# Kernel tuning notes

Measured on AMD Instinct MI355X. Metric: run time of the kernel, lower is better.

## Reference

```python
import jax, jax.numpy as jnp
import numpy as np

N = 10000       # n_nodes
E = 640000      # n_edges (avg degree 64)
D_IN = 128      # in_feats
D_H = 128       # n_hidden
N_CLS = 64      # n_classes


def setup_inputs() -> dict:
    key = jax.random.key(0)
    k1, k2, k3, k4, k5, k6 = jax.random.split(key, 6)
    features = jax.random.normal(k1, (N, D_IN), dtype=jnp.float32)
    src = jax.random.randint(k2, (E,), 0, N, dtype=jnp.int32)
    dst = jax.random.randint(k3, (E,), 0, N, dtype=jnp.int32)
    s = 0.05  # small init scale to keep activations bounded across 3 layers
    # Stored as [in, out]; equivalent to torch Linear weight [out, in] transposed.
    W0 = jax.random.normal(k4, (D_IN, D_H), dtype=jnp.float32) * s
    W1 = jax.random.normal(k5, (D_H, D_H), dtype=jnp.float32) * s
    W2 = jax.random.normal(k6, (D_H, N_CLS), dtype=jnp.float32) * s
    return {"features": features, "W0": W0, "W1": W1, "W2": W2,
            "src": src, "dst": dst}


def reference(features, W0, W1, W2, src, dst):
    # GINConv with aggregator 'sum', eps=0 (learn_eps=False):
    #   h' = Linear(h + sum_{(u->v) in E} h[u] scattered to v)
    # Dropout is identity at inference; 'activation' is unused in the module.
    def gin_layer(h, W):
        agg = jax.ops.segment_sum(h[src], dst, num_segments=N)  # [N, d]
        return (h + agg) @ W

    h = gin_layer(features, W0)
    h = gin_layer(h, W1)
    h = gin_layer(h, W2)
    return h
```

## Files before the change

kernel.cpp:

```cpp
#include <hip/hip_runtime.h>
#include <hip/hip_bf16.h>

#define NN 10000
#define NE 640000
#define D_IN 128
#define D_H 128
#define N_CLS 64
#define CAP 160
#define GRP 157
#define CAPC 4800
#define EPB 1024
#define AB 625
#define CB 1251
#define WB 80
#define CCS 16

__device__ __forceinline__ float blo(unsigned u) { return __uint_as_float(u << 16); }
__device__ __forceinline__ float bhi(unsigned u) { return __uint_as_float(u & 0xffff0000u); }
__device__ __forceinline__ unsigned short f2bf(float f) {
    unsigned u = __float_as_uint(f);
    return (unsigned short)((u + 0x7fffu + ((u >> 16) & 1u)) >> 16);
}
__device__ __forceinline__ unsigned packbf(float a, float b) {
    return (unsigned)f2bf(a) | ((unsigned)f2bf(b) << 16);
}

__global__ __launch_bounds__(256) void prep_a(const int* __restrict__ src,
                                              const int* __restrict__ dst,
                                              int* __restrict__ coarse_cnt,
                                              unsigned* __restrict__ coarse,
                                              const float* __restrict__ feat,
                                              unsigned* __restrict__ hb0,
                                              const float* __restrict__ W0,
                                              const float* __restrict__ W1,
                                              const float* __restrict__ W2,
                                              unsigned* __restrict__ wb0,
                                              unsigned* __restrict__ wb1,
                                              unsigned* __restrict__ wb2) {
    int bid = blockIdx.x;
    if (bid >= AB + CB) {
        int t = (bid - AB - CB) * 256 + threadIdx.x;
        if (t < 8192) {
            int kp = t >> 7, j = t & 127;
            wb0[t] = packbf(W0[(2 * kp) * 128 + j], W0[(2 * kp + 1) * 128 + j]);
        } else if (t < 16384) {
            int tt = t - 8192;
            int kp = tt >> 7, j = tt & 127;
            wb1[tt] = packbf(W1[(2 * kp) * 128 + j], W1[(2 * kp + 1) * 128 + j]);
        } else if (t < 20480) {
            int tt = t - 16384;
            int kp = tt >> 6, j = tt & 63;
            wb2[tt] = packbf(W2[(2 * kp) * 64 + j], W2[(2 * kp + 1) * 64 + j]);
        }
        return;
    }
    if (bid >= AB) {
        int t = (bid - AB) * 256 + threadIdx.x;
        if (t < NN * 32) {
            float4 f = ((const float4*)feat)[t];
            ((uint2*)hb0)[t] = make_uint2(packbf(f.x, f.y), packbf(f.z, f.w));
        } else if (t < (NN + 1) * 32) {
            ((uint2*)hb0)[t] = make_uint2(0u, 0u);
        }
        return;
    }
    __shared__ unsigned stage[EPB];
    __shared__ int hist[GRP], gbase[GRP], cur[GRP];
    const int t = threadIdx.x;
    for (int i = t; i < GRP; i += 256) hist[i] = 0;
    __syncthreads();
    const int e0 = bid * EPB;
    for (int i = t; i < EPB; i += 256) {
        int s = src[e0 + i];
        int d = dst[e0 + i];
        stage[i] = (unsigned)s | ((unsigned)d << 16);
        atomicAdd(&hist[d >> 6], 1);
    }
    __syncthreads();
    for (int i = t; i < GRP; i += 256) {
        gbase[i] = atomicAdd(&coarse_cnt[i * CCS], hist[i]);
        cur[i] = 0;
    }
    __syncthreads();
    for (int i = t; i < EPB; i += 256) {
        unsigned u = stage[i];
        int g = u >> 22;
        int r = atomicAdd(&cur[g], 1);
        coarse[g * CAPC + gbase[g] + r] = u;
    }
}

__global__ __launch_bounds__(1024) void prep_b(const int* __restrict__ coarse_cnt,
                                               const unsigned* __restrict__ coarse,
                                               int* __restrict__ cnt,
                                               unsigned short* __restrict__ colbuf) {
    __shared__ int cur[64];
    const int g = blockIdx.x;
    const int t = threadIdx.x;
    if (t < 64) cur[t] = 0;
    __syncthreads();
    const int m = coarse_cnt[g * CCS];
    const unsigned* cb = coarse + g * CAPC;
    for (int i = t; i < m; i += 1024) {
        unsigned u = cb[i];
        int s = (int)(u & 0xFFFFu);
        int d = (int)(u >> 16);
        int r = atomicAdd(&cur[d - (g << 6)], 1);
        colbuf[d * CAP + r] = (unsigned short)s;
    }
    __syncthreads();
    if (t < 64) {
        int n = (g << 6) + t;
        if (n < NN) {
            int c = cur[t];
            int pad = (16 - (c & 15)) & 15;
            unsigned short* base = colbuf + n * CAP;
            for (int k = 0; k < pad; ++k) base[c + k] = (unsigned short)NN;
            cnt[n] = c + pad;
        }
    }
}

template <int J, bool LAST>
__global__ __launch_bounds__(256, 8) void gin_layer(const uint4* __restrict__ hb4,
                                                    const int* __restrict__ cnt,
                                                    const unsigned short* __restrict__ colbuf,
                                                    const unsigned* __restrict__ Wb,
                                                    unsigned short* __restrict__ outb,
                                                    float* __restrict__ outf) {
    constexpr int M = 4;
    __shared__ float xs[M][D_H];
    const int base = blockIdx.x * M;
    const int tid = threadIdx.x;
    const int wave = tid >> 6;
    const int lane = tid & 63;
    const int sub = lane >> 4;
    const int off = lane & 15;

    const int n = base + wave;
    float a0, a1, a2, a3, a4, a5, a6, a7;
    if (sub == 0) {
        uint4 u = hb4[n * 16 + off];
        a0 = blo(u.x); a1 = bhi(u.x); a2 = blo(u.y); a3 = bhi(u.y);
        a4 = blo(u.z); a5 = bhi(u.z); a6 = blo(u.w); a7 = bhi(u.w);
    } else {
        a0 = a1 = a2 = a3 = a4 = a5 = a6 = a7 = 0.f;
    }
    const int G4 = cnt[n] >> 2;
    const uint2* cl8 = (const uint2*)(colbuf + n * CAP);
    for (int g = 0; g < G4; g += 4) {
        uint2 p0 = cl8[g + 0];
        uint2 p1 = cl8[g + 1];
        uint2 p2 = cl8[g + 2];
        uint2 p3 = cl8[g + 3];
        unsigned w0 = (sub & 2) ? p0.y : p0.x;
        unsigned w1 = (sub & 2) ? p1.y : p1.x;
        unsigned w2 = (sub & 2) ? p2.y : p2.x;
        unsigned w3 = (sub & 2) ? p3.y : p3.x;
        int s0 = (sub & 1) ? (w0 >> 16) : (w0 & 0xffffu);
        int s1 = (sub & 1) ? (w1 >> 16) : (w1 & 0xffffu);
        int s2 = (sub & 1) ? (w2 >> 16) : (w2 & 0xffffu);
        int s3 = (sub & 1) ? (w3 >> 16) : (w3 & 0xffffu);
        uint4 uA = hb4[s0 * 16 + off];
        uint4 uB = hb4[s1 * 16 + off];
        uint4 uC = hb4[s2 * 16 + off];
        uint4 uD = hb4[s3 * 16 + off];
        a0 += (blo(uA.x) + blo(uB.x)) + (blo(uC.x) + blo(uD.x));
        a1 += (bhi(uA.x) + bhi(uB.x)) + (bhi(uC.x) + bhi(uD.x));
        a2 += (blo(uA.y) + blo(uB.y)) + (blo(uC.y) + blo(uD.y));
        a3 += (bhi(uA.y) + bhi(uB.y)) + (bhi(uC.y) + bhi(uD.y));
        a4 += (blo(uA.z) + blo(uB.z)) + (blo(uC.z) + blo(uD.z));
        a5 += (bhi(uA.z) + bhi(uB.z)) + (bhi(uC.z) + bhi(uD.z));
        a6 += (blo(uA.w) + blo(uB.w)) + (blo(uC.w) + blo(uD.w));
        a7 += (bhi(uA.w) + bhi(uB.w)) + (bhi(uC.w) + bhi(uD.w));
    }
    a0 += __shfl_xor(a0, 16); a0 += __shfl_xor(a0, 32);
    a1 += __shfl_xor(a1, 16); a1 += __shfl_xor(a1, 32);
    a2 += __shfl_xor(a2, 16); a2 += __shfl_xor(a2, 32);
    a3 += __shfl_xor(a3, 16); a3 += __shfl_xor(a3, 32);
    a4 += __shfl_xor(a4, 16); a4 += __shfl_xor(a4, 32);
    a5 += __shfl_xor(a5, 16); a5 += __shfl_xor(a5, 32);
    a6 += __shfl_xor(a6, 16); a6 += __shfl_xor(a6, 32);
    a7 += __shfl_xor(a7, 16); a7 += __shfl_xor(a7, 32);
    if (sub == 0) {
        *(float4*)&xs[wave][8 * off]     = make_float4(a0, a1, a2, a3);
        *(float4*)&xs[wave][8 * off + 4] = make_float4(a4, a5, a6, a7);
    }
    __syncthreads();

    constexpr int G = 256 / J;
    constexpr int NM = M / G;
    const int gq = tid / J;
    const int j = tid % J;
    const int mbase = gq * NM;
    float acc[NM];
#pragma unroll
    for (int m = 0; m < NM; ++m) acc[m] = 0.f;

    for (int k = 0; k < D_H; k += 4) {
        unsigned wp0 = Wb[(k >> 1) * J + j];
        unsigned wp1 = Wb[((k >> 1) + 1) * J + j];
        float w0 = blo(wp0), w1 = bhi(wp0), w2 = blo(wp1), w3 = bhi(wp1);
#pragma unroll
        for (int m = 0; m < NM; ++m) {
            float4 xv = *(const float4*)&xs[mbase + m][k];
            acc[m] += xv.x * w0 + xv.y * w1 + xv.z * w2 + xv.w * w3;
        }
    }
#pragma unroll
    for (int m = 0; m < NM; ++m) {
        int n2 = base + mbase + m;
        if (LAST) __builtin_nontemporal_store(acc[m], &outf[(size_t)n2 * J + j]);
        else      __builtin_nontemporal_store(f2bf(acc[m]), &outb[(size_t)n2 * J + j]);
    }
    if (!LAST && blockIdx.x == 0 && tid < 32) {
        ((uint2*)(outb + (size_t)NN * D_H))[tid] = make_uint2(0u, 0u);
    }
}

extern "C" void kernel_launch(void* const* d_in, const int* in_sizes, int n_in,
                              void* d_out, int out_size, void* d_ws, size_t ws_size,
                              hipStream_t stream) {
    const float* features = (const float*)d_in[0];
    const float* W0       = (const float*)d_in[1];
    const float* W1       = (const float*)d_in[2];
    const float* W2       = (const float*)d_in[3];
    const int*   src      = (const int*)d_in[4];
    const int*   dst      = (const int*)d_in[5];
    float* out = (float*)d_out;

    int* coarse_cnt        = (int*)d_ws;
    int* cnt               = coarse_cnt + GRP * CCS;
    unsigned short* colbuf = (unsigned short*)(cnt + NN);
    unsigned* coarse       = (unsigned*)(colbuf + (size_t)NN * CAP);
    unsigned* hb0          = coarse + (size_t)GRP * CAPC;
    unsigned* hb1          = hb0 + (size_t)(NN + 1) * 64;
    unsigned* hb2          = hb1 + (size_t)(NN + 1) * 64;
    unsigned* wb0          = hb2 + (size_t)(NN + 1) * 64;
    unsigned* wb1          = wb0 + 8192;
    unsigned* wb2          = wb1 + 8192;

    hipMemsetAsync(coarse_cnt, 0, GRP * CCS * sizeof(int), stream);
    prep_a<<<AB + CB + WB, 256, 0, stream>>>(src, dst, coarse_cnt, coarse, features, hb0,
                                             W0, W1, W2, wb0, wb1, wb2);
    prep_b<<<GRP, 1024, 0, stream>>>(coarse_cnt, coarse, cnt, colbuf);

    gin_layer<D_H, false><<<NN / 4, 256, 0, stream>>>((const uint4*)hb0, cnt, colbuf, wb0,
                                                      (unsigned short*)hb1, nullptr);
    gin_layer<D_H, false><<<NN / 4, 256, 0, stream>>>((const uint4*)hb1, cnt, colbuf, wb1,
                                                      (unsigned short*)hb2, nullptr);
    gin_layer<N_CLS, true><<<NN / 4, 256, 0, stream>>>((const uint4*)hb2, cnt, colbuf, wb2,
                                                       nullptr, out);
}
```

Before: 148.4 us.

## Fuse CSR build and three GIN layers into one cooperative persistent kernel

Replaces the five separate launches (two prep kernels plus three layer kernels) with a single cooperative kernel of 768 persistent blocks that uses grid-wide syncs between phases. The fine bucketing step now spreads each coarse group across four blocks and uses global atomics on the per-node counts, with the column buffer pre-filled with the sentinel instead of padding each row. The aim is to remove launch gaps and tail effects between the short phases. In exchange it adds grid barrier costs and global atomic contention, and caps occupancy at 4 blocks per CU. If cooperative launch is unavailable it falls back to the old multi-kernel path.

New measurement: 151.8 us. 2.3% more time.

```diff
diff --git a/kernel.cpp b/kernel.cpp
--- a/kernel.cpp
+++ b/kernel.cpp
@@ -1,5 +1,8 @@
 #include <hip/hip_runtime.h>
 #include <hip/hip_bf16.h>
+#include <hip/hip_cooperative_groups.h>
+
+namespace cg = cooperative_groups;
 
 #define NN 10000
 #define NE 640000
@@ -9,11 +12,19 @@
 #define CAP 160
 #define GRP 157
 #define CAPC 4800
-#define EPB 1024
-#define AB 625
-#define CB 1251
-#define WB 80
 #define CCS 16
+#define SENT 10000
+
+#define F_EPB 1024
+#define F_AB 625
+#define F_CB 1251
+#define F_WB 80
+
+#define C_NB 768
+#define C_T 256
+#define C_EPB 834
+#define C_SL 4
+#define C_NPI 3072
 
 __device__ __forceinline__ float blo(unsigned u) { return __uint_as_float(u << 16); }
 __device__ __forceinline__ float bhi(unsigned u) { return __uint_as_float(u & 0xffff0000u); }
@@ -24,6 +35,7 @@
 __device__ __forceinline__ unsigned packbf(float a, float b) {
     return (unsigned)f2bf(a) | ((unsigned)f2bf(b) << 16);
 }
+
 
 __global__ __launch_bounds__(256) void prep_a(const int* __restrict__ src,
                                               const int* __restrict__ dst,
@@ -38,24 +50,22 @@
                                               unsigned* __restrict__ wb1,
                                               unsigned* __restrict__ wb2) {
     int bid = blockIdx.x;
-    if (bid >= AB + CB) {
-        int t = (bid - AB - CB) * 256 + threadIdx.x;
+    if (bid >= F_AB + F_CB) {
+        int t = (bid - F_AB - F_CB) * 256 + threadIdx.x;
         if (t < 8192) {
             int kp = t >> 7, j = t & 127;
             wb0[t] = packbf(W0[(2 * kp) * 128 + j], W0[(2 * kp + 1) * 128 + j]);
         } else if (t < 16384) {
-            int tt = t - 8192;
-            int kp = tt >> 7, j = tt & 127;
+            int tt = t - 8192, kp = tt >> 7, j = tt & 127;
             wb1[tt] = packbf(W1[(2 * kp) * 128 + j], W1[(2 * kp + 1) * 128 + j]);
         } else if (t < 20480) {
-            int tt = t - 16384;
-            int kp = tt >> 6, j = tt & 63;
+            int tt = t - 16384, kp = tt >> 6, j = tt & 63;
             wb2[tt] = packbf(W2[(2 * kp) * 64 + j], W2[(2 * kp + 1) * 64 + j]);
         }
         return;
     }
-    if (bid >= AB) {
-        int t = (bid - AB) * 256 + threadIdx.x;
+    if (bid >= F_AB) {
+        int t = (bid - F_AB) * 256 + threadIdx.x;
         if (t < NN * 32) {
             float4 f = ((const float4*)feat)[t];
             ((uint2*)hb0)[t] = make_uint2(packbf(f.x, f.y), packbf(f.z, f.w));
@@ -64,13 +74,13 @@
         }
         return;
     }
-    __shared__ unsigned stage[EPB];
+    __shared__ unsigned stage[F_EPB];
     __shared__ int hist[GRP], gbase[GRP], cur[GRP];
     const int t = threadIdx.x;
     for (int i = t; i < GRP; i += 256) hist[i] = 0;
     __syncthreads();
-    const int e0 = bid * EPB;
-    for (int i = t; i < EPB; i += 256) {
+    const int e0 = bid * F_EPB;
+    for (int i = t; i < F_EPB; i += 256) {
         int s = src[e0 + i];
         int d = dst[e0 + i];
         stage[i] = (unsigned)s | ((unsigned)d << 16);
@@ -82,7 +92,7 @@
         cur[i] = 0;
     }
     __syncthreads();
-    for (int i = t; i < EPB; i += 256) {
+    for (int i = t; i < F_EPB; i += 256) {
         unsigned u = stage[i];
         int g = u >> 22;
         int r = atomicAdd(&cur[g], 1);
@@ -115,7 +125,7 @@
             int c = cur[t];
             int pad = (16 - (c & 15)) & 15;
             unsigned short* base = colbuf + n * CAP;
-            for (int k = 0; k < pad; ++k) base[c + k] = (unsigned short)NN;
+            for (int k = 0; k < pad; ++k) base[c + k] = (unsigned short)SENT;
             cnt[n] = c + pad;
         }
     }
@@ -196,7 +206,6 @@
     float acc[NM];
 #pragma unroll
     for (int m = 0; m < NM; ++m) acc[m] = 0.f;
-
     for (int k = 0; k < D_H; k += 4) {
         unsigned wp0 = Wb[(k >> 1) * J + j];
         unsigned wp1 = Wb[((k >> 1) + 1) * J + j];
@@ -214,41 +223,256 @@
         else      __builtin_nontemporal_store(f2bf(acc[m]), &outb[(size_t)n2 * J + j]);
     }
     if (!LAST && blockIdx.x == 0 && tid < 32) {
-        ((uint2*)(outb + (size_t)NN * D_H))[tid] = make_uint2(0u, 0u);
-    }
-}
+        ((uint2*)(outb + (size_t)SENT * D_H))[tid] = make_uint2(0u, 0u);
+    }
+}
+
+
+struct Args {
+    const int* src; const int* dst;
+    int* coarse_cnt; unsigned* coarse;
+    const float* feat;
+    unsigned* hb0; unsigned* hb1; unsigned* hb2;
+    const float* W0; const float* W1; const float* W2;
+    unsigned* wb0; unsigned* wb1; unsigned* wb2;
+    int* cnt; unsigned short* colbuf;
+    float* out;
+};
+
+template <int J, bool LAST>
+__device__ __forceinline__ void layer_c(const uint4* __restrict__ hb4,
+                                        const int* __restrict__ cnt,
+                                        const unsigned short* __restrict__ colbuf,
+                                        const unsigned* __restrict__ Wb,
+                                        unsigned short* outb, float* outf,
+                                        float (*xs)[D_H], int b, int t) {
+    const int wave = t >> 6, lane = t & 63, sub = lane >> 4, off = lane & 15;
+#pragma unroll 1
+    for (int it = 0; it < 4; ++it) {
+        const int n = it * C_NPI + b * 4 + wave;
+        const bool valid = n < NN;
+        const int row = valid ? n : SENT;
+        float a0, a1, a2, a3, a4, a5, a6, a7;
+        if (sub == 0) {
+            uint4 u = hb4[row * 16 + off];
+            a0 = blo(u.x); a1 = bhi(u.x); a2 = blo(u.y); a3 = bhi(u.y);
+            a4 = blo(u.z); a5 = bhi(u.z); a6 = blo(u.w); a7 = bhi(u.w);
+        } else {
+            a0 = a1 = a2 = a3 = a4 = a5 = a6 = a7 = 0.f;
+        }
+        const int c = valid ? cnt[n] : 0;
+        const int iters = (c + 15) >> 4;
+        const uint2* cl8 = (const uint2*)(colbuf + (size_t)row * CAP);
+        for (int q = 0; q < iters; ++q) {
+            const int g = q * 4;
+            uint2 p0 = cl8[g + 0];
+            uint2 p1 = cl8[g + 1];
+            uint2 p2 = cl8[g + 2];
+            uint2 p3 = cl8[g + 3];
+            unsigned w0 = (sub & 2) ? p0.y : p0.x;
+            unsigned w1 = (sub & 2) ? p1.y : p1.x;
+            unsigned w2 = (sub & 2) ? p2.y : p2.x;
+            unsigned w3 = (sub & 2) ? p3.y : p3.x;
+            int s0 = (sub & 1) ? (w0 >> 16) : (w0 & 0xffffu);
+            int s1 = (sub & 1) ? (w1 >> 16) : (w1 & 0xffffu);
+            int s2 = (sub & 1) ? (w2 >> 16) : (w2 & 0xffffu);
+            int s3 = (sub & 1) ? (w3 >> 16) : (w3 & 0xffffu);
+            uint4 uA = hb4[s0 * 16 + off];
+            uint4 uB = hb4[s1 * 16 + off];
+            uint4 uC = hb4[s2 * 16 + off];
+            uint4 uD = hb4[s3 * 16 + off];
+            a0 += (blo(uA.x) + blo(uB.x)) + (blo(uC.x) + blo(uD.x));
+            a1 += (bhi(uA.x) + bhi(uB.x)) + (bhi(uC.x) + bhi(uD.x));
+            a2 += (blo(uA.y) + blo(uB.y)) + (blo(uC.y) + blo(uD.y));
+            a3 += (bhi(uA.y) + bhi(uB.y)) + (bhi(uC.y) + bhi(uD.y));
+            a4 += (blo(uA.z) + blo(uB.z)) + (blo(uC.z) + blo(uD.z));
+            a5 += (bhi(uA.z) + bhi(uB.z)) + (bhi(uC.z) + bhi(uD.z));
+            a6 += (blo(uA.w) + blo(uB.w)) + (blo(uC.w) + blo(uD.w));
+            a7 += (bhi(uA.w) + bhi(uB.w)) + (bhi(uC.w) + bhi(uD.w));
+        }
+        a0 += __shfl_xor(a0, 16); a0 += __shfl_xor(a0, 32);
+        a1 += __shfl_xor(a1, 16); a1 += __shfl_xor(a1, 32);
+        a2 += __shfl_xor(a2, 16); a2 += __shfl_xor(a2, 32);
+        a3 += __shfl_xor(a3, 16); a3 += __shfl_xor(a3, 32);
+        a4 += __shfl_xor(a4, 16); a4 += __shfl_xor(a4, 32);
+        a5 += __shfl_xor(a5, 16); a5 += __shfl_xor(a5, 32);
+        a6 += __shfl_xor(a6, 16); a6 += __shfl_xor(a6, 32);
+        a7 += __shfl_xor(a7, 16); a7 += __shfl_xor(a7, 32);
+        if (sub == 0) {
+            *(float4*)&xs[wave][8 * off]     = make_float4(a0, a1, a2, a3);
+            *(float4*)&xs[wave][8 * off + 4] = make_float4(a4, a5, a6, a7);
+        }
+        __syncthreads();
+
+        constexpr int G = 256 / J;
+        constexpr int NM = 4 / G;
+        const int gq = t / J;
+        const int j = t % J;
+        const int mbase = gq * NM;
+        float acc[NM];
+#pragma unroll
+        for (int m = 0; m < NM; ++m) acc[m] = 0.f;
+        for (int k = 0; k < D_H; k += 4) {
+            unsigned wp0 = Wb[(k >> 1) * J + j];
+            unsigned wp1 = Wb[((k >> 1) + 1) * J + j];
+            float w0 = blo(wp0), w1 = bhi(wp0), w2 = blo(wp1), w3 = bhi(wp1);
+#pragma unroll
+            for (int m = 0; m < NM; ++m) {
+                float4 xv = *(const float4*)&xs[mbase + m][k];
+                acc[m] += xv.x * w0 + xv.y * w1 + xv.z * w2 + xv.w * w3;
+            }
+        }
+#pragma unroll
+        for (int m = 0; m < NM; ++m) {
+            int n2 = it * C_NPI + b * 4 + mbase + m;
+            if (n2 < NN) {
+                if (LAST) __builtin_nontemporal_store(acc[m], &outf[(size_t)n2 * J + j]);
+                else      __builtin_nontemporal_store(f2bf(acc[m]), &outb[(size_t)n2 * J + j]);
+            }
+        }
+        if (!LAST && it == 0 && b == 0 && t < 32) {
+            ((uint2*)(outb + (size_t)SENT * D_H))[t] = make_uint2(0u, 0u);
+        }
+        __syncthreads();
+    }
+}
+
+__global__ __launch_bounds__(256, 4) void mega(Args a) {
+    cg::grid_group grid = cg::this_grid();
+    __shared__ unsigned stage[C_EPB];
+    __shared__ int hist[GRP], gbase[GRP], cur[GRP];
+    __shared__ float xs[4][D_H];
+    const int b = blockIdx.x;
+    const int t = threadIdx.x;
+    const int gtid = b * C_T + t;
+    const int NBT = C_NB * C_T;
+
+    for (int i = t; i < GRP; i += C_T) hist[i] = 0;
+    __syncthreads();
+    const int e0 = b * C_EPB;
+    const int ecnt = min(C_EPB, NE - e0);
+    for (int i = t; i < ecnt; i += C_T) {
+        int s = a.src[e0 + i];
+        int d = a.dst[e0 + i];
+        stage[i] = (unsigned)s | ((unsigned)d << 16);
+        atomicAdd(&hist[d >> 6], 1);
+    }
+    __syncthreads();
+    for (int i = t; i < GRP; i += C_T) {
+        gbase[i] = atomicAdd(&a.coarse_cnt[i * CCS], hist[i]);
+        cur[i] = 0;
+    }
+    __syncthreads();
+    for (int i = t; i < ecnt; i += C_T) {
+        unsigned u = stage[i];
+        int g = u >> 22;
+        int r = atomicAdd(&cur[g], 1);
+        a.coarse[g * CAPC + gbase[g] + r] = u;
+    }
+    for (int i = gtid; i < (NN + 1) * 32; i += NBT) {
+        if (i < NN * 32) {
+            float4 f = ((const float4*)a.feat)[i];
+            ((uint2*)a.hb0)[i] = make_uint2(packbf(f.x, f.y), packbf(f.z, f.w));
+        } else {
+            ((uint2*)a.hb0)[i] = make_uint2(0u, 0u);
+        }
+    }
+    if (gtid < 8192) {
+        int kp = gtid >> 7, j = gtid & 127;
+        a.wb0[gtid] = packbf(a.W0[(2 * kp) * 128 + j], a.W0[(2 * kp + 1) * 128 + j]);
+    } else if (gtid < 16384) {
+        int tt = gtid - 8192, kp = tt >> 7, j = tt & 127;
+        a.wb1[tt] = packbf(a.W1[(2 * kp) * 128 + j], a.W1[(2 * kp + 1) * 128 + j]);
+    } else if (gtid < 20480) {
+        int tt = gtid - 16384, kp = tt >> 6, j = tt & 63;
+        a.wb2[tt] = packbf(a.W2[(2 * kp) * 64 + j], a.W2[(2 * kp + 1) * 64 + j]);
+    }
+    if (gtid < 2500) ((int4*)a.cnt)[gtid] = make_int4(0, 0, 0, 0);
+    {
+        const uint4 sv = make_uint4(0x27102710u, 0x27102710u, 0x27102710u, 0x27102710u);
+        for (int i = gtid; i < NN * CAP / 8; i += NBT) ((uint4*)a.colbuf)[i] = sv;
+    }
+    __threadfence();
+    grid.sync();
+
+    if (b < GRP * C_SL) {
+        const int g = b / C_SL, sl = b % C_SL;
+        const int m = a.coarse_cnt[g * CCS];
+        const int lo = (int)((long long)m * sl / C_SL);
+        const int hi = (int)((long long)m * (sl + 1) / C_SL);
+        const unsigned* cb = a.coarse + g * CAPC;
+        for (int i = lo + t; i < hi; i += C_T) {
+            unsigned u = cb[i];
+            int s = (int)(u & 0xffffu);
+            int d = (int)(u >> 16);
+            int r = atomicAdd(&a.cnt[d], 1);
+            a.colbuf[(size_t)d * CAP + r] = (unsigned short)s;
+        }
+    }
+    __threadfence();
+    grid.sync();
+
+    layer_c<D_H, false>((const uint4*)a.hb0, a.cnt, a.colbuf, a.wb0,
+                        (unsigned short*)a.hb1, nullptr, xs, b, t);
+    __threadfence();
+    grid.sync();
+    layer_c<D_H, false>((const uint4*)a.hb1, a.cnt, a.colbuf, a.wb1,
+                        (unsigned short*)a.hb2, nullptr, xs, b, t);
+    __threadfence();
+    grid.sync();
+    layer_c<N_CLS, true>((const uint4*)a.hb2, a.cnt, a.colbuf, a.wb2,
+                         nullptr, a.out, xs, b, t);
+}
+
 
 extern "C" void kernel_launch(void* const* d_in, const int* in_sizes, int n_in,
                               void* d_out, int out_size, void* d_ws, size_t ws_size,
                               hipStream_t stream) {
-    const float* features = (const float*)d_in[0];
-    const float* W0       = (const float*)d_in[1];
-    const float* W1       = (const float*)d_in[2];
-    const float* W2       = (const float*)d_in[3];
-    const int*   src      = (const int*)d_in[4];
-    const int*   dst      = (const int*)d_in[5];
-    float* out = (float*)d_out;
-
-    int* coarse_cnt        = (int*)d_ws;
-    int* cnt               = coarse_cnt + GRP * CCS;
-    unsigned short* colbuf = (unsigned short*)(cnt + NN);
-    unsigned* coarse       = (unsigned*)(colbuf + (size_t)NN * CAP);
-    unsigned* hb0          = coarse + (size_t)GRP * CAPC;
-    unsigned* hb1          = hb0 + (size_t)(NN + 1) * 64;
-    unsigned* hb2          = hb1 + (size_t)(NN + 1) * 64;
-    unsigned* wb0          = hb2 + (size_t)(NN + 1) * 64;
-    unsigned* wb1          = wb0 + 8192;
-    unsigned* wb2          = wb1 + 8192;
-
-    hipMemsetAsync(coarse_cnt, 0, GRP * CCS * sizeof(int), stream);
-    prep_a<<<AB + CB + WB, 256, 0, stream>>>(src, dst, coarse_cnt, coarse, features, hb0,
-                                             W0, W1, W2, wb0, wb1, wb2);
-    prep_b<<<GRP, 1024, 0, stream>>>(coarse_cnt, coarse, cnt, colbuf);
-
-    gin_layer<D_H, false><<<NN / 4, 256, 0, stream>>>((const uint4*)hb0, cnt, colbuf, wb0,
-                                                      (unsigned short*)hb1, nullptr);
-    gin_layer<D_H, false><<<NN / 4, 256, 0, stream>>>((const uint4*)hb1, cnt, colbuf, wb1,
-                                                      (unsigned short*)hb2, nullptr);
-    gin_layer<N_CLS, true><<<NN / 4, 256, 0, stream>>>((const uint4*)hb2, cnt, colbuf, wb2,
-                                                       nullptr, out);
-}
+    Args a;
+    a.feat = (const float*)d_in[0];
+    a.W0   = (const float*)d_in[1];
+    a.W1   = (const float*)d_in[2];
+    a.W2   = (const float*)d_in[3];
+    a.src  = (const int*)d_in[4];
+    a.dst  = (const int*)d_in[5];
+    a.out  = (float*)d_out;
+
+    a.coarse_cnt = (int*)d_ws;
+    a.cnt        = a.coarse_cnt + GRP * CCS;
+    a.colbuf     = (unsigned short*)(a.cnt + NN + 8);
+    a.coarse     = (unsigned*)(a.colbuf + (size_t)NN * CAP);
+    a.hb0        = a.coarse + (size_t)GRP * CAPC;
+    a.hb1        = a.hb0 + (size_t)(NN + 1) * 64;
+    a.hb2        = a.hb1 + (size_t)(NN + 1) * 64;
+    a.wb0        = a.hb2 + (size_t)(NN + 1) * 64;
+    a.wb1        = a.wb0 + 8192;
+    a.wb2        = a.wb1 + 8192;
+
+    hipMemsetAsync(a.coarse_cnt, 0, GRP * CCS * sizeof(int), stream);
+
+    int dev = 0;
+    hipGetDevice(&dev);
+    int coop = 0, ncu = 0, maxblk = 0;
+    hipDeviceGetAttribute(&coop, hipDeviceAttributeCooperativeLaunch, dev);
+    hipDeviceGetAttribute(&ncu, hipDeviceAttributeMultiprocessorCount, dev);
+    hipOccupancyMaxActiveBlocksPerMultiprocessor(&maxblk, (const void*)mega, C_T, 0);
+
+    if (coop && (long long)maxblk * ncu >= C_NB) {
+        void* params[] = { &a };
+        hipError_t e = hipLaunchCooperativeKernel((const void*)mega, dim3(C_NB), dim3(C_T),
+                                                  params, 0, stream);
+        if (e == hipSuccess) return;
+        (void)hipGetLastError();
+    }
+
+    prep_a<<<F_AB + F_CB + F_WB, 256, 0, stream>>>(a.src, a.dst, a.coarse_cnt, a.coarse,
+                                                   a.feat, a.hb0, a.W0, a.W1, a.W2,
+                                                   a.wb0, a.wb1, a.wb2);
+    prep_b<<<GRP, 1024, 0, stream>>>(a.coarse_cnt, a.coarse, a.cnt, a.colbuf);
+    gin_layer<D_H, false><<<NN / 4, 256, 0, stream>>>((const uint4*)a.hb0, a.cnt, a.colbuf,
+                                                      a.wb0, (unsigned short*)a.hb1, nullptr);
+    gin_layer<D_H, false><<<NN / 4, 256, 0, stream>>>((const uint4*)a.hb1, a.cnt, a.colbuf,
+                                                      a.wb1, (unsigned short*)a.hb2, nullptr);
+    gin_layer<N_CLS, true><<<NN / 4, 256, 0, stream>>>((const uint4*)a.hb2, a.cnt, a.colbuf,
+                                                       a.wb2, nullptr, a.out);
+}
```
